# Performance work log

Measured on AMD Instinct MI355X. Metric: run time of the kernel, lower is better.

Reference implementation:

```python
import jax, jax.numpy as jnp
import numpy as np

N_HEAD = 16
N_BLOCKS = 2
EPS = 1e-6

def _rmsnorm(x, g):
    return x * jax.lax.rsqrt(jnp.mean(x * x, axis=-1, keepdims=True) + EPS) * g

def _causal_sa(x, Wqkv, Wproj, g):
    # x: (B, T, C); fused qkv, RMSNorm on q/k over full C before head split
    B, T, C = x.shape
    hd = C // N_HEAD
    q, k, v = jnp.split(x @ Wqkv, 3, axis=-1)
    q = _rmsnorm(q, g)
    k = _rmsnorm(k, g)
    def heads(t):
        return t.reshape(B, T, N_HEAD, hd).transpose(0, 2, 1, 3)
    q, k, v = heads(q), heads(k), heads(v)
    scores = jnp.einsum('bhqd,bhkd->bhqk', q, k) * (1.0 / np.sqrt(hd))
    mask = jnp.tril(jnp.ones((T, T), dtype=bool))
    scores = jnp.where(mask, scores, -jnp.finfo(scores.dtype).max)
    att = jax.nn.softmax(scores, axis=-1)
    y = jnp.einsum('bhqk,bhkd->bhqd', att, v)
    y = y.transpose(0, 2, 1, 3).reshape(B, T, C)
    return y @ Wproj

def setup_inputs() -> dict:
    key = jax.random.key(0)
    ks = jax.random.split(key, 8)
    B, ng, T, C = 2, 8, 256, 1024
    M_loc, M_glob = 16, 16
    s = 0.02
    return {
        'x': jax.random.normal(ks[0], (B, ng, T, C), jnp.float32),
        'mem_tokens': jax.random.normal(ks[1], (B, M_glob, C), jnp.float32),
        'local_mem': jax.random.normal(ks[2], (B, ng, M_loc, C), jnp.float32),
        'Wqkv_loc': jax.random.normal(ks[3], (N_BLOCKS, C, 3 * C), jnp.float32) * s,
        'Wproj_loc': jax.random.normal(ks[4], (N_BLOCKS, C, C), jnp.float32) * s,
        'g_loc': jnp.ones((N_BLOCKS, C), jnp.float32),
        'Wqkv_glob': jax.random.normal(ks[5], (N_BLOCKS, C, 3 * C), jnp.float32) * s,
        'Wproj_glob': jax.random.normal(ks[6], (N_BLOCKS, C, C), jnp.float32) * s,
        'g_glob': jnp.ones((N_BLOCKS, C), jnp.float32),
    }

def reference(x, mem_tokens, local_mem, Wqkv_loc, Wproj_loc, g_loc, Wqkv_glob, Wproj_glob, g_glob):
    B, ng, T, C = x.shape
    M_loc = local_mem.shape[2]
    M_glob = mem_tokens.shape[1]
    for i in range(N_BLOCKS):
        # local causal SA: per-group, with local mem tokens prepended
        xl = jnp.concatenate([local_mem, x], axis=2).reshape(B * ng, M_loc + T, C)
        yl = _causal_sa(xl, Wqkv_loc[i], Wproj_loc[i], g_loc[i])
        yl = yl.reshape(B, ng, M_loc + T, C)
        local_mem = yl[:, :, :M_loc, :]
        x = yl[:, :, M_loc:, :]
        # global causal SA over flattened sequence with global mem tokens
        xg = x.reshape(B, ng * T, C)
        xg = jnp.concatenate([mem_tokens, xg], axis=1)
        yg = _causal_sa(xg, Wqkv_glob[i], Wproj_glob[i], g_glob[i])
        mem_tokens = yg[:, :M_glob, :]
        x = yg[:, M_glob:, :].reshape(B, ng, T, C)
    return x
```

## Files before the change

kernel.cpp:

```cpp
#include <hip/hip_runtime.h>
#include <hip/hip_bf16.h>
#include <math.h>

typedef __attribute__((ext_vector_type(8))) short s16x8;
typedef __attribute__((ext_vector_type(4))) short s16x4;
typedef __attribute__((ext_vector_type(4))) float f32x4;

#define MPAD 4352
#define LG 2064
#define CT 8
#define SM_SHIFT 11.5415603f
#define PS_LD 80

__device__ __forceinline__ short f2b(float f) {
  unsigned u = __float_as_uint(f);
  unsigned r = (u + 0x7fffu + ((u >> 16) & 1u)) >> 16;
  return (short)(unsigned short)r;
}
__device__ __forceinline__ short f2b_fast(float f) {
  return (short)((__float_as_uint(f) + 0x8000u) >> 16);
}
__device__ __forceinline__ float b2f(short s) {
  return __uint_as_float(((unsigned)(unsigned short)s) << 16);
}
__device__ __forceinline__ float fexp2(float x) {
#if __has_builtin(__builtin_amdgcn_exp2f)
  return __builtin_amdgcn_exp2f(x);
#else
  float r;
  asm("v_exp_f32 %0, %1" : "=v"(r) : "v"(x));
  return r;
#endif
}

__device__ __forceinline__ void gl_lds16(const short* g, short* l) {
  __builtin_amdgcn_global_load_lds((const __attribute__((address_space(1))) short*)g,
                                   (__attribute__((address_space(3))) short*)l, 16, 0, 0);
}

__global__ __launch_bounds__(256) void transpose_cast(const float* __restrict__ in,
                                                      short* __restrict__ out,
                                                      int K, int N) {
  __shared__ float tile[32][33];
  int bn = blockIdx.x * 32;
  int bk = blockIdx.y * 32;
  for (int i = threadIdx.y; i < 32; i += 8)
    tile[i][threadIdx.x] = in[(size_t)(bk + i) * N + bn + threadIdx.x];
  __syncthreads();
  for (int i = threadIdx.y; i < 32; i += 8)
    out[(size_t)(bn + i) * K + bk + threadIdx.x] = f2b(tile[threadIdx.x][i]);
}

__global__ __launch_bounds__(256) void transpose_v(const short* __restrict__ QKV,
                                                   short* __restrict__ Vt,
                                                   int L, int Lpad) {
  __shared__ short tile[32][33];
  int sh = blockIdx.z;
  int s = sh >> 4, h = sh & 15;
  int kb = blockIdx.x * 32;
  int cb = blockIdx.y * 32;
  int tx = threadIdx.x;
  for (int i = threadIdx.y; i < 32; i += 8) {
    int key = kb + i;
    if (key > L - 1) key = L - 1;
    tile[i][tx] = QKV[(size_t)(s * L + key) * 3072 + 2048 + h * 64 + cb + tx];
  }
  __syncthreads();
  for (int i = threadIdx.y; i < 32; i += 8)
    Vt[((size_t)sh * 64 + cb + i) * Lpad + kb + tx] = tile[tx][i];
}

__global__ __launch_bounds__(256) void gemm_bt3(const short* __restrict__ A,
                                                const short* __restrict__ BT,
                                                short* __restrict__ C,
                                                int K, int N) {
  __shared__ short As[2][128 * 32];
  __shared__ short Bs[2][128 * 32];
  const int tid = threadIdx.x;
  const int lane = tid & 63;
  const int w = tid >> 6;
  const int wr = (w >> 1) * 64, wc = (w & 1) * 64;
  const int m0 = blockIdx.y * 128;
  const int n0 = blockIdx.x * 128;
  const int l15 = lane & 15, lhi = lane >> 4;

  f32x4 acc[4][4] = {};

  auto STAGE = [&](int b, int k0) {
#pragma unroll
    for (int p = 0; p < 2; ++p) {
      int g = w * 128 + p * 64 + lane;
      int row = g >> 2;
      int cs = (g & 3) * 8;
      gl_lds16(A + (size_t)(m0 + row) * K + k0 + cs, &As[b][g * 8]);
      gl_lds16(BT + (size_t)(n0 + row) * K + k0 + cs, &Bs[b][g * 8]);
    }
  };

  const int nt = K >> 5;
  STAGE(0, 0);
  __syncthreads();
  int cur = 0;
  for (int t = 0; t < nt; ++t) {
    if (t + 1 < nt) STAGE(cur ^ 1, (t + 1) << 5);
    s16x8 af[4], bf[4];
#pragma unroll
    for (int m = 0; m < 4; ++m)
      af[m] = *(const s16x8*)(&As[cur][(wr + m * 16 + l15) * 32 + lhi * 8]);
#pragma unroll
    for (int n = 0; n < 4; ++n)
      bf[n] = *(const s16x8*)(&Bs[cur][(wc + n * 16 + l15) * 32 + lhi * 8]);
#pragma unroll
    for (int m = 0; m < 4; ++m)
#pragma unroll
      for (int n = 0; n < 4; ++n)
        acc[m][n] = __builtin_amdgcn_mfma_f32_16x16x32_bf16(af[m], bf[n], acc[m][n], 0, 0, 0);
    __syncthreads();
    cur ^= 1;
  }
#pragma unroll
  for (int m = 0; m < 4; ++m) {
    int row_base = m0 + wr + m * 16 + lhi * 4;
#pragma unroll
    for (int n = 0; n < 4; ++n) {
      int col = n0 + wc + n * 16 + l15;
#pragma unroll
      for (int r = 0; r < 4; ++r)
        C[(size_t)(row_base + r) * N + col] = f2b(acc[m][n][r]);
    }
  }
}

__global__ __launch_bounds__(256) void rmsnorm_qk(short* __restrict__ QKV,
                                                  const float* __restrict__ g) {
  int row = blockIdx.x;
  int which = blockIdx.y;
  size_t base = (size_t)row * 3072 + (size_t)which * 1024;
  int t = threadIdx.x;
  s16x4 in = *(const s16x4*)(QKV + base + t * 4);
  float v[4];
  float ss = 0.f;
#pragma unroll
  for (int j = 0; j < 4; ++j) {
    v[j] = b2f(in[j]);
    ss += v[j] * v[j];
  }
#pragma unroll
  for (int m = 32; m >= 1; m >>= 1) ss += __shfl_xor(ss, m);
  __shared__ float red[4];
  if ((t & 63) == 0) red[t >> 6] = ss;
  __syncthreads();
  float tot = red[0] + red[1] + red[2] + red[3];
  float inv = rsqrtf(tot * (1.0f / 1024.0f) + 1e-6f);
  if (which == 0) inv *= 0.125f * 1.44269504f;
  s16x4 out;
#pragma unroll
  for (int j = 0; j < 4; ++j) out[j] = f2b(v[j] * inv * g[t * 4 + j]);
  *(s16x4*)(&QKV[base + t * 4]) = out;
}

__global__ __launch_bounds__(256) void attn_causal3(const short* __restrict__ QKV,
                                                    const short* __restrict__ Vt,
                                                    short* __restrict__ Y,
                                                    int L, int Lpad) {
  const int h = blockIdx.y, s = blockIdx.z;
  const int q0 = blockIdx.x * 64;
  const int tid = threadIdx.x;
  const int lane = tid & 63, w = tid >> 6;
  const int l15 = lane & 15, lhi = lane >> 4;
  const int row0 = s * L;

  __shared__ short Ks[64][72];
  __shared__ short Vs[2][64][72];
  __shared__ short Ps[4][16][PS_LD];

  int qld = q0 + w * 16 + l15;
  if (qld > L - 1) qld = L - 1;
  const size_t qrow = (size_t)(row0 + qld) * 3072 + h * 64;
  s16x8 qf0 = *(const s16x8*)(QKV + qrow + lhi * 8);
  s16x8 qf1 = *(const s16x8*)(QKV + qrow + 32 + lhi * 8);

  float lsum[4] = {0.f, 0.f, 0.f, 0.f};
  f32x4 o[4];
#pragma unroll
  for (int d = 0; d < 4; ++d) o[d] = f32x4{0.f, 0.f, 0.f, 0.f};

  const short* Vbase = Vt + (size_t)(s * 16 + h) * 64 * Lpad;

  s16x8 kreg[2], vreg[2];
#pragma unroll
  for (int p = 0; p < 2; ++p) {
    int g = tid + p * 256;
    int kr = g >> 3, cs = (g & 7) * 8;
    int krow = kr;
    if (krow > L - 1) krow = L - 1;
    kreg[p] = *(const s16x8*)(QKV + (size_t)(row0 + krow) * 3072 + 1024 + h * 64 + cs);
    vreg[p] = *(const s16x8*)(Vbase + (size_t)kr * Lpad + cs);
  }

  int buf = 0;
  for (int kb = 0; kb <= q0; kb += 64, buf ^= 1) {
#pragma unroll
    for (int p = 0; p < 2; ++p) {
      int g = tid + p * 256;
      int kr = g >> 3, cs = (g & 7) * 8;
      *(s16x8*)(&Ks[kr][cs]) = kreg[p];
      *(s16x8*)(&Vs[buf][kr][cs]) = vreg[p];
    }
    if (kb + 64 <= q0) {
#pragma unroll
      for (int p = 0; p < 2; ++p) {
        int g = tid + p * 256;
        int kr = g >> 3, cs = (g & 7) * 8;
        int krow = kb + 64 + kr;
        if (krow > L - 1) krow = L - 1;
        kreg[p] = *(const s16x8*)(QKV + (size_t)(row0 + krow) * 3072 + 1024 + h * 64 + cs);
        vreg[p] = *(const s16x8*)(Vbase + (size_t)kr * Lpad + kb + 64 + cs);
      }
    }
    __syncthreads();

    f32x4 st[4];
#pragma unroll
    for (int n = 0; n < 4; ++n) {
      s16x8 k0 = *(const s16x8*)(&Ks[n * 16 + l15][lhi * 8]);
      s16x8 k1 = *(const s16x8*)(&Ks[n * 16 + l15][32 + lhi * 8]);
      f32x4 sa = f32x4{-SM_SHIFT, -SM_SHIFT, -SM_SHIFT, -SM_SHIFT};
      sa = __builtin_amdgcn_mfma_f32_16x16x32_bf16(qf0, k0, sa, 0, 0, 0);
      sa = __builtin_amdgcn_mfma_f32_16x16x32_bf16(qf1, k1, sa, 0, 0, 0);
      st[n] = sa;
    }

    if (kb == q0) {
#pragma unroll
      for (int n = 0; n < 4; ++n) {
        int key = kb + n * 16 + l15;
#pragma unroll
        for (int r = 0; r < 4; ++r) {
          int qr = q0 + w * 16 + lhi * 4 + r;
          if (key > qr) st[n][r] = -1e30f;
        }
      }
    }

#pragma unroll
    for (int n = 0; n < 4; ++n) {
#pragma unroll
      for (int r = 0; r < 4; ++r) {
        float p = fexp2(st[n][r]);
        Ps[w][lhi * 4 + r][n * 16 + l15] = f2b_fast(p);
        lsum[r] += p;
      }
    }
    __syncthreads();

#pragma unroll
    for (int kk = 0; kk < 2; ++kk) {
      s16x8 pa = *(const s16x8*)(&Ps[w][l15][kk * 32 + lhi * 8]);
#pragma unroll
      for (int d = 0; d < 4; ++d) {
        s16x8 vf = *(const s16x8*)(&Vs[buf][d * 16 + l15][kk * 32 + lhi * 8]);
        o[d] = __builtin_amdgcn_mfma_f32_16x16x32_bf16(pa, vf, o[d], 0, 0, 0);
      }
    }
  }

#pragma unroll
  for (int r = 0; r < 4; ++r) {
#pragma unroll
    for (int mm = 1; mm <= 8; mm <<= 1) lsum[r] += __shfl_xor(lsum[r], mm, 16);
  }
#pragma unroll
  for (int d = 0; d < 4; ++d) {
#pragma unroll
    for (int r = 0; r < 4; ++r) {
      int qr = q0 + w * 16 + lhi * 4 + r;
      if (qr < L)
        Y[(size_t)(row0 + qr) * 1024 + h * 64 + d * 16 + l15] = f2b(o[d][r] / lsum[r]);
    }
  }
}

__global__ __launch_bounds__(256) void attn_split(const short* __restrict__ QKV,
                                                  const short* __restrict__ Vt,
                                                  float* __restrict__ o_acc,
                                                  float* __restrict__ ls_acc) {
  const int qb = blockIdx.x;
  const int chunk = blockIdx.y;
  const int sh = blockIdx.z;
  const int t0 = chunk * CT;
  if (t0 > qb) return;
  const int t1 = min(t0 + CT, qb + 1);
  const int h = sh & 15, s = sh >> 4;
  const int q0 = qb * 64;
  const int tid = threadIdx.x;
  const int lane = tid & 63, w = tid >> 6;
  const int l15 = lane & 15, lhi = lane >> 4;
  const int row0 = s * LG;
  const int Lpad = 2112;

  __shared__ short Ks[64][72];
  __shared__ short Vs[2][64][72];
  __shared__ short Ps[4][16][PS_LD];

  int qld = q0 + w * 16 + l15;
  if (qld > LG - 1) qld = LG - 1;
  const size_t qrow = (size_t)(row0 + qld) * 3072 + h * 64;
  s16x8 qf0 = *(const s16x8*)(QKV + qrow + lhi * 8);
  s16x8 qf1 = *(const s16x8*)(QKV + qrow + 32 + lhi * 8);

  float lsum[4] = {0.f, 0.f, 0.f, 0.f};
  f32x4 o[4];
#pragma unroll
  for (int d = 0; d < 4; ++d) o[d] = f32x4{0.f, 0.f, 0.f, 0.f};

  const short* Vbase = Vt + (size_t)sh * 64 * Lpad;

  s16x8 kreg[2], vreg[2];
  const int kb0 = t0 * 64;
#pragma unroll
  for (int p = 0; p < 2; ++p) {
    int g = tid + p * 256;
    int kr = g >> 3, cs = (g & 7) * 8;
    int krow = kb0 + kr;
    if (krow > LG - 1) krow = LG - 1;
    kreg[p] = *(const s16x8*)(QKV + (size_t)(row0 + krow) * 3072 + 1024 + h * 64 + cs);
    vreg[p] = *(const s16x8*)(Vbase + (size_t)kr * Lpad + kb0 + cs);
  }

  int buf = 0;
  for (int t = t0; t < t1; ++t, buf ^= 1) {
    const int kb = t * 64;
#pragma unroll
    for (int p = 0; p < 2; ++p) {
      int g = tid + p * 256;
      int kr = g >> 3, cs = (g & 7) * 8;
      *(s16x8*)(&Ks[kr][cs]) = kreg[p];
      *(s16x8*)(&Vs[buf][kr][cs]) = vreg[p];
    }
    if (t + 1 < t1) {
#pragma unroll
      for (int p = 0; p < 2; ++p) {
        int g = tid + p * 256;
        int kr = g >> 3, cs = (g & 7) * 8;
        int krow = kb + 64 + kr;
        if (krow > LG - 1) krow = LG - 1;
        kreg[p] = *(const s16x8*)(QKV + (size_t)(row0 + krow) * 3072 + 1024 + h * 64 + cs);
        vreg[p] = *(const s16x8*)(Vbase + (size_t)kr * Lpad + kb + 64 + cs);
      }
    }
    __syncthreads();

    f32x4 st[4];
#pragma unroll
    for (int n = 0; n < 4; ++n) {
      s16x8 k0 = *(const s16x8*)(&Ks[n * 16 + l15][lhi * 8]);
      s16x8 k1 = *(const s16x8*)(&Ks[n * 16 + l15][32 + lhi * 8]);
      f32x4 sa = f32x4{-SM_SHIFT, -SM_SHIFT, -SM_SHIFT, -SM_SHIFT};
      sa = __builtin_amdgcn_mfma_f32_16x16x32_bf16(qf0, k0, sa, 0, 0, 0);
      sa = __builtin_amdgcn_mfma_f32_16x16x32_bf16(qf1, k1, sa, 0, 0, 0);
      st[n] = sa;
    }

    if (t == qb) {
#pragma unroll
      for (int n = 0; n < 4; ++n) {
        int key = kb + n * 16 + l15;
#pragma unroll
        for (int r = 0; r < 4; ++r) {
          int qr = q0 + w * 16 + lhi * 4 + r;
          if (key > qr) st[n][r] = -1e30f;
        }
      }
    }

#pragma unroll
    for (int n = 0; n < 4; ++n) {
#pragma unroll
      for (int r = 0; r < 4; ++r) {
        float p = fexp2(st[n][r]);
        Ps[w][lhi * 4 + r][n * 16 + l15] = f2b_fast(p);
        lsum[r] += p;
      }
    }
    __syncthreads();

#pragma unroll
    for (int kk = 0; kk < 2; ++kk) {
      s16x8 pa = *(const s16x8*)(&Ps[w][l15][kk * 32 + lhi * 8]);
#pragma unroll
      for (int d = 0; d < 4; ++d) {
        s16x8 vf = *(const s16x8*)(&Vs[buf][d * 16 + l15][kk * 32 + lhi * 8]);
        o[d] = __builtin_amdgcn_mfma_f32_16x16x32_bf16(pa, vf, o[d], 0, 0, 0);
      }
    }
  }

#pragma unroll
  for (int r = 0; r < 4; ++r) {
#pragma unroll
    for (int mm = 1; mm <= 8; mm <<= 1) lsum[r] += __shfl_xor(lsum[r], mm, 16);
  }
#pragma unroll
  for (int r = 0; r < 4; ++r) {
    int qr = q0 + w * 16 + lhi * 4 + r;
    if (qr < LG) {
      if (l15 == 0) atomicAdd(&ls_acc[(size_t)sh * LG + qr], lsum[r]);
#pragma unroll
      for (int d = 0; d < 4; ++d)
        atomicAdd(&o_acc[((size_t)sh * LG + qr) * 64 + d * 16 + l15], o[d][r]);
    }
  }
}

__global__ __launch_bounds__(256) void attn_merge(const float* __restrict__ o_acc,
                                                  const float* __restrict__ ls_acc,
                                                  short* __restrict__ Y) {
  int sh = blockIdx.z * 16 + blockIdx.y;
  int s = sh >> 4, h = sh & 15;
  int row = blockIdx.x * 4 + (threadIdx.x >> 6);
  int col = threadIdx.x & 63;
  if (row < LG) {
    float inv = 1.0f / ls_acc[(size_t)sh * LG + row];
    float v = o_acc[((size_t)sh * LG + row) * 64 + col];
    Y[(size_t)(s * LG + row) * 1024 + h * 64 + col] = f2b(v * inv);
  }
}

__global__ __launch_bounds__(256) void build_xl(const float* __restrict__ x,
                                                const float* __restrict__ lm,
                                                short* __restrict__ Xin) {
  int row = blockIdx.x;
  int s = row / 272, r = row % 272;
  const float* src = (r < 16) ? lm + ((size_t)s * 16 + r) * 1024
                              : x + ((size_t)s * 256 + (r - 16)) * 1024;
  int t = threadIdx.x;
  f32x4 v = *(const f32x4*)(src + t * 4);
  s16x4 o;
#pragma unroll
  for (int j = 0; j < 4; ++j) o[j] = f2b(v[j]);
  *(s16x4*)(&Xin[(size_t)row * 1024 + t * 4]) = o;
}

__global__ __launch_bounds__(256) void split_local_build_xg(const short* __restrict__ Pout,
                                                            const float* __restrict__ mem_src,
                                                            float* __restrict__ lm_out,
                                                            short* __restrict__ Xin) {
  int row = blockIdx.x;
  int t = threadIdx.x;
  if (row < 4352) {
    int sr = row < 4128 ? row : 4127;
    int b = sr / 2064, r = sr % 2064;
    s16x4 o;
    if (r < 16) {
      f32x4 v = *(const f32x4*)(mem_src + ((size_t)(b * 16 + r)) * 1024 + t * 4);
#pragma unroll
      for (int j = 0; j < 4; ++j) o[j] = f2b(v[j]);
    } else {
      int f = b * 2048 + (r - 16);
      int pr = (f >> 8) * 272 + 16 + (f & 255);
      o = *(const s16x4*)(Pout + (size_t)pr * 1024 + t * 4);
    }
    *(s16x4*)(&Xin[(size_t)row * 1024 + t * 4]) = o;
  } else {
    int m = row - 4352;
    int pr = (m >> 4) * 272 + (m & 15);
    s16x4 v = *(const s16x4*)(Pout + (size_t)pr * 1024 + t * 4);
    f32x4 o;
#pragma unroll
    for (int j = 0; j < 4; ++j) o[j] = b2f(v[j]);
    *(f32x4*)(&lm_out[(size_t)m * 1024 + t * 4]) = o;
  }
}

__global__ __launch_bounds__(256) void split_global_build_xl(const short* __restrict__ Pout,
                                                             const float* __restrict__ lm_src,
                                                             float* __restrict__ mem_out,
                                                             short* __restrict__ Xin) {
  int row = blockIdx.x;
  int t = threadIdx.x;
  if (row < 4352) {
    int s = row / 272, r = row % 272;
    s16x4 o;
    if (r < 16) {
      f32x4 v = *(const f32x4*)(lm_src + ((size_t)(s * 16 + r)) * 1024 + t * 4);
#pragma unroll
      for (int j = 0; j < 4; ++j) o[j] = f2b(v[j]);
    } else {
      int f = s * 256 + (r - 16);
      int pr = (f >> 11) * 2064 + 16 + (f & 2047);
      o = *(const s16x4*)(Pout + (size_t)pr * 1024 + t * 4);
    }
    *(s16x4*)(&Xin[(size_t)row * 1024 + t * 4]) = o;
  } else {
    int m = row - 4352;
    int pr = (m >> 4) * 2064 + (m & 15);
    s16x4 v = *(const s16x4*)(Pout + (size_t)pr * 1024 + t * 4);
    f32x4 o;
#pragma unroll
    for (int j = 0; j < 4; ++j) o[j] = b2f(v[j]);
    *(f32x4*)(&mem_out[(size_t)m * 1024 + t * 4]) = o;
  }
}

__global__ __launch_bounds__(256) void split_global_final(const short* __restrict__ Pout,
                                                          float* __restrict__ out) {
  int f = blockIdx.x;
  int t = threadIdx.x;
  int pr = (f >> 11) * 2064 + 16 + (f & 2047);
  s16x4 v = *(const s16x4*)(Pout + (size_t)pr * 1024 + t * 4);
  f32x4 o;
#pragma unroll
  for (int j = 0; j < 4; ++j) o[j] = b2f(v[j]);
  *(f32x4*)(&out[(size_t)f * 1024 + t * 4]) = o;
}

extern "C" void kernel_launch(void* const* d_in, const int* in_sizes, int n_in,
                              void* d_out, int out_size, void* d_ws, size_t ws_size,
                              hipStream_t stream) {
  const float* x_in = (const float*)d_in[0];
  const float* mem_in = (const float*)d_in[1];
  const float* lm_in = (const float*)d_in[2];
  const float* Wqkv_loc = (const float*)d_in[3];
  const float* Wproj_loc = (const float*)d_in[4];
  const float* g_loc = (const float*)d_in[5];
  const float* Wqkv_glob = (const float*)d_in[6];
  const float* Wproj_glob = (const float*)d_in[7];
  const float* g_glob = (const float*)d_in[8];

  char* ws = (char*)d_ws;
  size_t off = 0;
  auto alloc = [&](size_t bytes) {
    char* p = ws + off;
    off += (bytes + 255) & ~(size_t)255;
    return p;
  };
  short* Wt = (short*)alloc((size_t)3072 * 1024 * 2);
  float* lm_cur = (float*)alloc((size_t)256 * 1024 * 4);
  float* mem_cur = (float*)alloc((size_t)32 * 1024 * 4);
  short* Xin = (short*)alloc((size_t)MPAD * 1024 * 2);
  short* QKVb = (short*)alloc((size_t)MPAD * 3072 * 2);
  short* Yb = (short*)alloc((size_t)MPAD * 1024 * 2);
  short* Pout = (short*)alloc((size_t)MPAD * 1024 * 2);
  short* Vtb = (short*)alloc((size_t)256 * 64 * 320 * 2);
  size_t oacc_bytes = (size_t)32 * LG * 64 * 4;
  size_t lacc_bytes = (size_t)32 * LG * 4;
  float* o_acc = (float*)alloc(oacc_bytes);
  float* ls_acc = (float*)alloc(lacc_bytes);
  const bool use_split = (ws_size >= off);

  for (int i = 0; i < 2; ++i) {
    transpose_cast<<<dim3(96, 32), dim3(32, 8), 0, stream>>>(
        Wqkv_loc + (size_t)i * 1024 * 3072, Wt, 1024, 3072);
    if (i == 0) build_xl<<<4352, 256, 0, stream>>>(x_in, lm_in, Xin);
    gemm_bt3<<<dim3(24, 34), 256, 0, stream>>>(Xin, Wt, QKVb, 1024, 3072);
    rmsnorm_qk<<<dim3(4352, 2), 256, 0, stream>>>(QKVb, g_loc + (size_t)i * 1024);
    transpose_v<<<dim3(10, 2, 256), dim3(32, 8), 0, stream>>>(QKVb, Vtb, 272, 320);
    attn_causal3<<<dim3(5, 16, 16), 256, 0, stream>>>(QKVb, Vtb, Yb, 272, 320);
    transpose_cast<<<dim3(32, 32), dim3(32, 8), 0, stream>>>(
        Wproj_loc + (size_t)i * 1024 * 1024, Wt, 1024, 1024);
    gemm_bt3<<<dim3(8, 34), 256, 0, stream>>>(Yb, Wt, Pout, 1024, 1024);
    split_local_build_xg<<<4608, 256, 0, stream>>>(Pout, i == 0 ? mem_in : mem_cur,
                                                   lm_cur, Xin);

    transpose_cast<<<dim3(96, 32), dim3(32, 8), 0, stream>>>(
        Wqkv_glob + (size_t)i * 1024 * 3072, Wt, 1024, 3072);
    gemm_bt3<<<dim3(24, 34), 256, 0, stream>>>(Xin, Wt, QKVb, 1024, 3072);
    rmsnorm_qk<<<dim3(4128, 2), 256, 0, stream>>>(QKVb, g_glob + (size_t)i * 1024);
    transpose_v<<<dim3(66, 2, 32), dim3(32, 8), 0, stream>>>(QKVb, Vtb, 2064, 2112);
    if (use_split) {
      hipMemsetAsync(o_acc, 0, oacc_bytes, stream);
      hipMemsetAsync(ls_acc, 0, lacc_bytes, stream);
      attn_split<<<dim3(33, 5, 32), 256, 0, stream>>>(QKVb, Vtb, o_acc, ls_acc);
      attn_merge<<<dim3(516, 16, 2), 256, 0, stream>>>(o_acc, ls_acc, Yb);
    } else {
      attn_causal3<<<dim3(33, 16, 2), 256, 0, stream>>>(QKVb, Vtb, Yb, 2064, 2112);
    }
    transpose_cast<<<dim3(32, 32), dim3(32, 8), 0, stream>>>(
        Wproj_glob + (size_t)i * 1024 * 1024, Wt, 1024, 1024);
    gemm_bt3<<<dim3(8, 34), 256, 0, stream>>>(Yb, Wt, Pout, 1024, 1024);
    if (i == 0)
      split_global_build_xl<<<4384, 256, 0, stream>>>(Pout, lm_cur, mem_cur, Xin);
    else
      split_global_final<<<4096, 256, 0, stream>>>(Pout, (float*)d_out);
  }
}
```

Before: 593.4 us.

## Keep attention probabilities in registers via transposed QK^T and lane shuffles

New measurement: 590.2 us. Within noise of the previous version (-0.6%).

```diff
diff --git a/kernel.cpp b/kernel.cpp
--- a/kernel.cpp
+++ b/kernel.cpp
@@ -10,15 +10,11 @@
 #define LG 2064
 #define CT 8
 #define SM_SHIFT 11.5415603f
-#define PS_LD 80
 
 __device__ __forceinline__ short f2b(float f) {
   unsigned u = __float_as_uint(f);
   unsigned r = (u + 0x7fffu + ((u >> 16) & 1u)) >> 16;
   return (short)(unsigned short)r;
-}
-__device__ __forceinline__ short f2b_fast(float f) {
-  return (short)((__float_as_uint(f) + 0x8000u) >> 16);
 }
 __device__ __forceinline__ float b2f(short s) {
   return __uint_as_float(((unsigned)(unsigned short)s) << 16);
@@ -31,6 +27,11 @@
   asm("v_exp_f32 %0, %1" : "=v"(r) : "v"(x));
   return r;
 #endif
+}
+__device__ __forceinline__ int cvtpk(float lo, float hi) {
+  int r;
+  asm("v_cvt_pk_bf16_f32 %0, %1, %2" : "=v"(r) : "v"(lo), "v"(hi));
+  return r;
 }
 
 __device__ __forceinline__ void gl_lds16(const short* g, short* l) {
@@ -159,7 +160,8 @@
   *(s16x4*)(&QKV[base + t * 4]) = out;
 }
 
-__global__ __launch_bounds__(256) void attn_causal3(const short* __restrict__ QKV,
+
+__global__ __launch_bounds__(256) void attn_causal4(const short* __restrict__ QKV,
                                                     const short* __restrict__ Vt,
                                                     short* __restrict__ Y,
                                                     int L, int Lpad) {
@@ -170,9 +172,8 @@
   const int l15 = lane & 15, lhi = lane >> 4;
   const int row0 = s * L;
 
-  __shared__ short Ks[64][72];
+  __shared__ short Ks[2][64][72];
   __shared__ short Vs[2][64][72];
-  __shared__ short Ps[4][16][PS_LD];
 
   int qld = q0 + w * 16 + l15;
   if (qld > L - 1) qld = L - 1;
@@ -180,12 +181,15 @@
   s16x8 qf0 = *(const s16x8*)(QKV + qrow + lhi * 8);
   s16x8 qf1 = *(const s16x8*)(QKV + qrow + 32 + lhi * 8);
 
-  float lsum[4] = {0.f, 0.f, 0.f, 0.f};
+  float lsum = 0.f;
   f32x4 o[4];
 #pragma unroll
   for (int d = 0; d < 4; ++d) o[d] = f32x4{0.f, 0.f, 0.f, 0.f};
 
   const short* Vbase = Vt + (size_t)(s * 16 + h) * 64 * Lpad;
+  const int sA = (lhi & 1) * 32 + l15;
+  const int sB = sA + 16;
+  const int bh = lhi >> 1;
 
   s16x8 kreg[2], vreg[2];
 #pragma unroll
@@ -204,9 +208,10 @@
     for (int p = 0; p < 2; ++p) {
       int g = tid + p * 256;
       int kr = g >> 3, cs = (g & 7) * 8;
-      *(s16x8*)(&Ks[kr][cs]) = kreg[p];
+      *(s16x8*)(&Ks[buf][kr][cs]) = kreg[p];
       *(s16x8*)(&Vs[buf][kr][cs]) = vreg[p];
     }
+    __syncthreads();
     if (kb + 64 <= q0) {
 #pragma unroll
       for (int p = 0; p < 2; ++p) {
@@ -218,45 +223,52 @@
         vreg[p] = *(const s16x8*)(Vbase + (size_t)kr * Lpad + kb + 64 + cs);
       }
     }
-    __syncthreads();
 
     f32x4 st[4];
 #pragma unroll
     for (int n = 0; n < 4; ++n) {
-      s16x8 k0 = *(const s16x8*)(&Ks[n * 16 + l15][lhi * 8]);
-      s16x8 k1 = *(const s16x8*)(&Ks[n * 16 + l15][32 + lhi * 8]);
+      s16x8 k0 = *(const s16x8*)(&Ks[buf][n * 16 + l15][lhi * 8]);
+      s16x8 k1 = *(const s16x8*)(&Ks[buf][n * 16 + l15][32 + lhi * 8]);
       f32x4 sa = f32x4{-SM_SHIFT, -SM_SHIFT, -SM_SHIFT, -SM_SHIFT};
-      sa = __builtin_amdgcn_mfma_f32_16x16x32_bf16(qf0, k0, sa, 0, 0, 0);
-      sa = __builtin_amdgcn_mfma_f32_16x16x32_bf16(qf1, k1, sa, 0, 0, 0);
+      sa = __builtin_amdgcn_mfma_f32_16x16x32_bf16(k0, qf0, sa, 0, 0, 0);
+      sa = __builtin_amdgcn_mfma_f32_16x16x32_bf16(k1, qf1, sa, 0, 0, 0);
       st[n] = sa;
     }
 
     if (kb == q0) {
+      int q = q0 + w * 16 + l15;
 #pragma unroll
       for (int n = 0; n < 4; ++n) {
-        int key = kb + n * 16 + l15;
 #pragma unroll
         for (int r = 0; r < 4; ++r) {
-          int qr = q0 + w * 16 + lhi * 4 + r;
-          if (key > qr) st[n][r] = -1e30f;
+          int key = kb + n * 16 + lhi * 4 + r;
+          if (key > q) st[n][r] = -1e30f;
         }
       }
     }
 
+    int wd[4][2];
 #pragma unroll
     for (int n = 0; n < 4; ++n) {
-#pragma unroll
-      for (int r = 0; r < 4; ++r) {
-        float p = fexp2(st[n][r]);
-        Ps[w][lhi * 4 + r][n * 16 + l15] = f2b_fast(p);
-        lsum[r] += p;
-      }
-    }
-    __syncthreads();
+      float p0 = fexp2(st[n][0]), p1 = fexp2(st[n][1]);
+      float p2 = fexp2(st[n][2]), p3 = fexp2(st[n][3]);
+      lsum += (p0 + p1) + (p2 + p3);
+      wd[n][0] = cvtpk(p0, p1);
+      wd[n][1] = cvtpk(p2, p3);
+    }
 
 #pragma unroll
     for (int kk = 0; kk < 2; ++kk) {
-      s16x8 pa = *(const s16x8*)(&Ps[w][l15][kk * 32 + lhi * 8]);
+      int a0 = __shfl(wd[2 * kk][0], sA), a1 = __shfl(wd[2 * kk][1], sA);
+      int a2 = __shfl(wd[2 * kk][0], sB), a3 = __shfl(wd[2 * kk][1], sB);
+      int b0 = __shfl(wd[2 * kk + 1][0], sA), b1 = __shfl(wd[2 * kk + 1][1], sA);
+      int b2 = __shfl(wd[2 * kk + 1][0], sB), b3 = __shfl(wd[2 * kk + 1][1], sB);
+      int pw[4];
+      pw[0] = bh ? b0 : a0;
+      pw[1] = bh ? b1 : a1;
+      pw[2] = bh ? b2 : a2;
+      pw[3] = bh ? b3 : a3;
+      s16x8 pa = *(const s16x8*)pw;
 #pragma unroll
       for (int d = 0; d < 4; ++d) {
         s16x8 vf = *(const s16x8*)(&Vs[buf][d * 16 + l15][kk * 32 + lhi * 8]);
@@ -265,26 +277,26 @@
     }
   }
 
-#pragma unroll
-  for (int r = 0; r < 4; ++r) {
-#pragma unroll
-    for (int mm = 1; mm <= 8; mm <<= 1) lsum[r] += __shfl_xor(lsum[r], mm, 16);
-  }
+  lsum += __shfl_xor(lsum, 16);
+  lsum += __shfl_xor(lsum, 32);
+  float lsq[4];
+#pragma unroll
+  for (int r = 0; r < 4; ++r) lsq[r] = __shfl(lsum, lhi * 4 + r);
 #pragma unroll
   for (int d = 0; d < 4; ++d) {
 #pragma unroll
     for (int r = 0; r < 4; ++r) {
       int qr = q0 + w * 16 + lhi * 4 + r;
       if (qr < L)
-        Y[(size_t)(row0 + qr) * 1024 + h * 64 + d * 16 + l15] = f2b(o[d][r] / lsum[r]);
-    }
-  }
-}
-
-__global__ __launch_bounds__(256) void attn_split(const short* __restrict__ QKV,
-                                                  const short* __restrict__ Vt,
-                                                  float* __restrict__ o_acc,
-                                                  float* __restrict__ ls_acc) {
+        Y[(size_t)(row0 + qr) * 1024 + h * 64 + d * 16 + l15] = f2b(o[d][r] / lsq[r]);
+    }
+  }
+}
+
+__global__ __launch_bounds__(256) void attn_split2(const short* __restrict__ QKV,
+                                                   const short* __restrict__ Vt,
+                                                   float* __restrict__ o_acc,
+                                                   float* __restrict__ ls_acc) {
   const int qb = blockIdx.x;
   const int chunk = blockIdx.y;
   const int sh = blockIdx.z;
@@ -299,9 +311,8 @@
   const int row0 = s * LG;
   const int Lpad = 2112;
 
-  __shared__ short Ks[64][72];
+  __shared__ short Ks[2][64][72];
   __shared__ short Vs[2][64][72];
-  __shared__ short Ps[4][16][PS_LD];
 
   int qld = q0 + w * 16 + l15;
   if (qld > LG - 1) qld = LG - 1;
@@ -309,12 +320,15 @@
   s16x8 qf0 = *(const s16x8*)(QKV + qrow + lhi * 8);
   s16x8 qf1 = *(const s16x8*)(QKV + qrow + 32 + lhi * 8);
 
-  float lsum[4] = {0.f, 0.f, 0.f, 0.f};
+  float lsum = 0.f;
   f32x4 o[4];
 #pragma unroll
   for (int d = 0; d < 4; ++d) o[d] = f32x4{0.f, 0.f, 0.f, 0.f};
 
   const short* Vbase = Vt + (size_t)sh * 64 * Lpad;
+  const int sA = (lhi & 1) * 32 + l15;
+  const int sB = sA + 16;
+  const int bh = lhi >> 1;
 
   s16x8 kreg[2], vreg[2];
   const int kb0 = t0 * 64;
@@ -335,9 +349,10 @@
     for (int p = 0; p < 2; ++p) {
       int g = tid + p * 256;
       int kr = g >> 3, cs = (g & 7) * 8;
-      *(s16x8*)(&Ks[kr][cs]) = kreg[p];
+      *(s16x8*)(&Ks[buf][kr][cs]) = kreg[p];
       *(s16x8*)(&Vs[buf][kr][cs]) = vreg[p];
     }
+    __syncthreads();
     if (t + 1 < t1) {
 #pragma unroll
       for (int p = 0; p < 2; ++p) {
@@ -349,45 +364,52 @@
         vreg[p] = *(const s16x8*)(Vbase + (size_t)kr * Lpad + kb + 64 + cs);
       }
     }
-    __syncthreads();
 
     f32x4 st[4];
 #pragma unroll
     for (int n = 0; n < 4; ++n) {
-      s16x8 k0 = *(const s16x8*)(&Ks[n * 16 + l15][lhi * 8]);
-      s16x8 k1 = *(const s16x8*)(&Ks[n * 16 + l15][32 + lhi * 8]);
+      s16x8 k0 = *(const s16x8*)(&Ks[buf][n * 16 + l15][lhi * 8]);
+      s16x8 k1 = *(const s16x8*)(&Ks[buf][n * 16 + l15][32 + lhi * 8]);
       f32x4 sa = f32x4{-SM_SHIFT, -SM_SHIFT, -SM_SHIFT, -SM_SHIFT};
-      sa = __builtin_amdgcn_mfma_f32_16x16x32_bf16(qf0, k0, sa, 0, 0, 0);
-      sa = __builtin_amdgcn_mfma_f32_16x16x32_bf16(qf1, k1, sa, 0, 0, 0);
+      sa = __builtin_amdgcn_mfma_f32_16x16x32_bf16(k0, qf0, sa, 0, 0, 0);
+      sa = __builtin_amdgcn_mfma_f32_16x16x32_bf16(k1, qf1, sa, 0, 0, 0);
       st[n] = sa;
     }
 
     if (t == qb) {
+      int q = q0 + w * 16 + l15;
 #pragma unroll
       for (int n = 0; n < 4; ++n) {
-        int key = kb + n * 16 + l15;
 #pragma unroll
         for (int r = 0; r < 4; ++r) {
-          int qr = q0 + w * 16 + lhi * 4 + r;
-          if (key > qr) st[n][r] = -1e30f;
+          int key = kb + n * 16 + lhi * 4 + r;
+          if (key > q) st[n][r] = -1e30f;
         }
       }
     }
 
+    int wd[4][2];
 #pragma unroll
     for (int n = 0; n < 4; ++n) {
-#pragma unroll
-      for (int r = 0; r < 4; ++r) {
-        float p = fexp2(st[n][r]);
-        Ps[w][lhi * 4 + r][n * 16 + l15] = f2b_fast(p);
-        lsum[r] += p;
-      }
-    }
-    __syncthreads();
+      float p0 = fexp2(st[n][0]), p1 = fexp2(st[n][1]);
+      float p2 = fexp2(st[n][2]), p3 = fexp2(st[n][3]);
+      lsum += (p0 + p1) + (p2 + p3);
+      wd[n][0] = cvtpk(p0, p1);
+      wd[n][1] = cvtpk(p2, p3);
+    }
 
 #pragma unroll
     for (int kk = 0; kk < 2; ++kk) {
-      s16x8 pa = *(const s16x8*)(&Ps[w][l15][kk * 32 + lhi * 8]);
+      int a0 = __shfl(wd[2 * kk][0], sA), a1 = __shfl(wd[2 * kk][1], sA);
+      int a2 = __shfl(wd[2 * kk][0], sB), a3 = __shfl(wd[2 * kk][1], sB);
+      int b0 = __shfl(wd[2 * kk + 1][0], sA), b1 = __shfl(wd[2 * kk + 1][1], sA);
+      int b2 = __shfl(wd[2 * kk + 1][0], sB), b3 = __shfl(wd[2 * kk + 1][1], sB);
+      int pw[4];
+      pw[0] = bh ? b0 : a0;
+      pw[1] = bh ? b1 : a1;
+      pw[2] = bh ? b2 : a2;
+      pw[3] = bh ? b3 : a3;
+      s16x8 pa = *(const s16x8*)pw;
 #pragma unroll
       for (int d = 0; d < 4; ++d) {
         s16x8 vf = *(const s16x8*)(&Vs[buf][d * 16 + l15][kk * 32 + lhi * 8]);
@@ -396,16 +418,14 @@
     }
   }
 
-#pragma unroll
-  for (int r = 0; r < 4; ++r) {
-#pragma unroll
-    for (int mm = 1; mm <= 8; mm <<= 1) lsum[r] += __shfl_xor(lsum[r], mm, 16);
-  }
+  lsum += __shfl_xor(lsum, 16);
+  lsum += __shfl_xor(lsum, 32);
+  int qmy = q0 + w * 16 + l15;
+  if (lhi == 0 && qmy < LG) atomicAdd(&ls_acc[(size_t)sh * LG + qmy], lsum);
 #pragma unroll
   for (int r = 0; r < 4; ++r) {
     int qr = q0 + w * 16 + lhi * 4 + r;
     if (qr < LG) {
-      if (l15 == 0) atomicAdd(&ls_acc[(size_t)sh * LG + qr], lsum[r]);
 #pragma unroll
       for (int d = 0; d < 4; ++d)
         atomicAdd(&o_acc[((size_t)sh * LG + qr) * 64 + d * 16 + l15], o[d][r]);
@@ -556,7 +576,7 @@
     gemm_bt3<<<dim3(24, 34), 256, 0, stream>>>(Xin, Wt, QKVb, 1024, 3072);
     rmsnorm_qk<<<dim3(4352, 2), 256, 0, stream>>>(QKVb, g_loc + (size_t)i * 1024);
     transpose_v<<<dim3(10, 2, 256), dim3(32, 8), 0, stream>>>(QKVb, Vtb, 272, 320);
-    attn_causal3<<<dim3(5, 16, 16), 256, 0, stream>>>(QKVb, Vtb, Yb, 272, 320);
+    attn_causal4<<<dim3(5, 16, 16), 256, 0, stream>>>(QKVb, Vtb, Yb, 272, 320);
     transpose_cast<<<dim3(32, 32), dim3(32, 8), 0, stream>>>(
         Wproj_loc + (size_t)i * 1024 * 1024, Wt, 1024, 1024);
     gemm_bt3<<<dim3(8, 34), 256, 0, stream>>>(Yb, Wt, Pout, 1024, 1024);
@@ -571,10 +591,10 @@
     if (use_split) {
       hipMemsetAsync(o_acc, 0, oacc_bytes, stream);
       hipMemsetAsync(ls_acc, 0, lacc_bytes, stream);
-      attn_split<<<dim3(33, 5, 32), 256, 0, stream>>>(QKVb, Vtb, o_acc, ls_acc);
+      attn_split2<<<dim3(33, 5, 32), 256, 0, stream>>>(QKVb, Vtb, o_acc, ls_acc);
       attn_merge<<<dim3(516, 16, 2), 256, 0, stream>>>(o_acc, ls_acc, Yb);
     } else {
-      attn_causal3<<<dim3(33, 16, 2), 256, 0, stream>>>(QKVb, Vtb, Yb, 2064, 2112);
+      attn_causal4<<<dim3(33, 16, 2), 256, 0, stream>>>(QKVb, Vtb, Yb, 2064, 2112);
     }
     transpose_cast<<<dim3(32, 32), dim3(32, 8), 0, stream>>>(
         Wproj_glob + (size_t)i * 1024 * 1024, Wt, 1024, 1024);
```
